# Performance work log

Measured on AMD Instinct MI355X. Metric: run time of the kernel, lower is better.

## Reference

```python
import jax, jax.numpy as jnp
import numpy as np

N_NODES = 100000
E_HALF = 500000   # undirected pairs; mirrored to E = 1M directed edges
NFEAT = 128
NHID = 64
NCLASS = 40


def setup_inputs() -> dict:
    key = jax.random.key(0)
    ks = jax.random.split(key, 8)
    s = jax.random.randint(ks[0], (E_HALF,), 0, N_NODES, dtype=jnp.int32)
    off = jax.random.randint(ks[1], (E_HALF,), 1, N_NODES, dtype=jnp.int32)
    d = (s + off) % N_NODES  # no self-loops in the raw edge list
    src = jnp.concatenate([s, d])
    dst = jnp.concatenate([d, s])
    ar = jnp.arange(E_HALF, dtype=jnp.int32)
    rev = jnp.concatenate([ar + E_HALF, ar])  # index of reverse edge (j,i) for edge (i,j)
    x = jax.random.uniform(ks[2], (N_NODES, NFEAT), dtype=jnp.float32)
    W1 = jax.random.normal(ks[3], (NFEAT, NHID), jnp.float32) / np.sqrt(NFEAT).astype(np.float32)
    b1 = jnp.zeros((NHID,), jnp.float32)
    W2 = jax.random.normal(ks[4], (NHID, NCLASS), jnp.float32) / np.sqrt(NHID).astype(np.float32)
    b2 = jnp.zeros((NCLASS,), jnp.float32)
    Wd = jax.random.normal(ks[5], (2, 1), jnp.float32)
    bd = jax.random.normal(ks[6], (1,), jnp.float32) * 0.1
    return {"x": x, "src": src, "dst": dst, "rev": rev,
            "W1": W1, "b1": b1, "W2": W2, "b2": b2, "Wd": Wd, "bd": bd}


def att_coef(f, src, dst, rev, n, Wd, bd, mask):
    """Edge-list version of GuardGCN.att_coef (drop=True).
    mask zeroes edges removed by a previous att_coef pass.
    Returns (per-edge weights [E], per-node self-loop weights [n])."""
    nrm = jnp.sqrt(jnp.sum(f * f, axis=1))
    safe = jnp.where(nrm == 0, 1.0, nrm)
    # cosine similarity only on the listed edges (diagonal handled via lam below)
    sim = jnp.sum(f[src] * f[dst], axis=1) / (safe[src] * safe[dst])
    sim = jnp.where(sim < 0.1, 0.0, sim) * mask
    # L1 row normalization (sklearn normalize(axis=1, norm='l1'))
    rowsum = jax.ops.segment_sum(jnp.abs(sim), src, num_segments=n)
    a = sim / jnp.where(rowsum == 0, 1.0, rowsum)[src]
    # learnable drop: Linear(2,1) on [a_ij, a_ji] -> sigmoid -> binary keep at 0.5
    char = jnp.stack([a, a[rev]], axis=1)  # [E, 2]
    keep = jax.nn.sigmoid(char @ Wd + bd)[:, 0] > 0.5
    a = jnp.where(keep, a, 0.0)
    # self-loop weight lam_i = 1 / (deg_i + 1), deg = surviving out-edges
    deg = jax.ops.segment_sum((a != 0).astype(f.dtype), src, num_segments=n)
    lam = 1.0 / (deg + 1.0)
    # exp() applied only to nonzero entries (zeros are absent in sparse nonzero())
    w_e = jnp.where(a > 0, jnp.exp(a), 0.0)
    w_s = jnp.exp(lam)
    return w_e, w_s


def gcn_conv(h, src, dst, w, n, W, b):
    """torch_geometric GCNConv: gcn_norm (add self-loops fill=1, sym D^-1/2 A D^-1/2),
    then aggregate h @ W along edges (src -> dst) and add bias."""
    h = h @ W
    iota = jnp.arange(n, dtype=src.dtype)
    src2 = jnp.concatenate([src, iota])
    dst2 = jnp.concatenate([dst, iota])
    w2 = jnp.concatenate([w, jnp.ones((n,), h.dtype)])
    deg = jax.ops.segment_sum(w2, dst2, num_segments=n)
    dis = jnp.where(deg > 0, deg ** -0.5, 0.0)
    norm = dis[src2] * w2 * dis[dst2]
    out = jax.ops.segment_sum(norm[:, None] * h[src2], dst2, num_segments=n)
    return out + b


def reference(x, src, dst, rev, W1, b1, W2, b2, Wd, bd):
    n = x.shape[0]
    iota = jnp.arange(n, dtype=src.dtype)
    # layer-0 attention on raw features
    w_e1, w_s1 = att_coef(x, src, dst, rev, n, Wd, bd, jnp.ones(src.shape, x.dtype))
    src_f = jnp.concatenate([src, iota])
    dst_f = jnp.concatenate([dst, iota])
    w_f1 = jnp.concatenate([w_e1, w_s1])
    h = jax.nn.relu(gcn_conv(x, src_f, dst_f, w_f1, n, W1, b1))
    # layer-1 attention on hidden features; edge set = survivors of pass 0
    mask1 = (w_e1 > 0).astype(x.dtype)
    w_e2, w_s2 = att_coef(h, src, dst, rev, n, Wd, bd, mask1)
    w_f2 = jnp.concatenate([w_e2, w_s2])
    # dropout is identity in eval mode
    out = gcn_conv(h, src_f, dst_f, w_f2, n, W2, b2)
    return jax.nn.log_softmax(out, axis=1)
```

## Files before the change

### kernel.cpp

```cpp
#include <hip/hip_runtime.h>

#define N_NODES 100000
#define E_HALF  500000
#define E_TOT   1000000
#define NFEAT   128
#define NHID    64
#define NCLS    40
#define NBUK    782
#define NSUB    8
#define CAP     448

__device__ __forceinline__ int REV(int e) { return (e < E_HALF) ? e + E_HALF : e - E_HALF; }

template<int D>
__global__ __launch_bounds__(256) void row_norm_k(const float* __restrict__ x, float* __restrict__ nrm) {
    int w = (blockIdx.x * 256 + threadIdx.x) >> 6;
    int lane = threadIdx.x & 63;
    if (w >= N_NODES) return;
    const float* row = x + (size_t)w * D;
    float s = 0.f;
#pragma unroll
    for (int i = 0; i < D / 64; ++i) { float v = row[lane + 64 * i]; s = fmaf(v, v, s); }
#pragma unroll
    for (int off = 32; off; off >>= 1) s += __shfl_xor(s, off);
    if (lane == 0) nrm[w] = sqrtf(s);
}

template<int D, int L, bool MASKED>
__global__ __launch_bounds__(256) void sim_k(const float* __restrict__ f, const float* __restrict__ nrm,
                                             const int* __restrict__ src, const int* __restrict__ dst,
                                             const float* __restrict__ we_mask,
                                             float* __restrict__ sim) {
    static_assert(D / L == 16, "each lane covers 16 floats");
    int g = blockIdx.x * 256 + threadIdx.x;
    int ep = g / L, sl = g % L;
    if (ep >= E_HALF) return;
    bool m0 = true, m1 = true;
    if (MASKED) {
        m0 = we_mask[ep] > 0.f;
        m1 = we_mask[ep + E_HALF] > 0.f;
        if (!m0 && !m1) {
            if (sl == 0) { sim[ep] = 0.f; sim[ep + E_HALF] = 0.f; }
            return;
        }
    }
    int s = src[ep], d = dst[ep];
    const float* fa = f + (size_t)s * D + sl * 16;
    const float* fb = f + (size_t)d * D + sl * 16;
    float acc = 0.f;
#pragma unroll
    for (int i = 0; i < 16; i += 4) {
        float4 va = *(const float4*)(fa + i);
        float4 vb = *(const float4*)(fb + i);
        acc = fmaf(va.x, vb.x, acc); acc = fmaf(va.y, vb.y, acc);
        acc = fmaf(va.z, vb.z, acc); acc = fmaf(va.w, vb.w, acc);
    }
#pragma unroll
    for (int off = L / 2; off; off >>= 1) acc += __shfl_xor(acc, off);
    if (sl == 0) {
        float na = nrm[s]; na = (na == 0.f) ? 1.f : na;
        float nb = nrm[d]; nb = (nb == 0.f) ? 1.f : nb;
        float c = acc / (na * nb);
        float t = (c < 0.1f) ? 0.f : c;
        sim[ep]          = m0 ? t : 0.f;
        sim[ep + E_HALF] = m1 ? t : 0.f;
    }
}

__global__ __launch_bounds__(256) void rowsum_k(const float* __restrict__ sim, const int* __restrict__ row_start,
                                                const int2* __restrict__ csr, float* __restrict__ rowsum) {
    int g = blockIdx.x * 256 + threadIdx.x;
    int j = g >> 2, l = g & 3;
    if (j >= N_NODES) return;
    int e0 = row_start[j], e1 = row_start[j + 1];
    float s = 0.f;
    for (int t = e0 + l; t < e1; t += 4) s += sim[csr[t].y];
    s += __shfl_xor(s, 1); s += __shfl_xor(s, 2);
    if (l == 0) rowsum[j] = s;
}

__global__ __launch_bounds__(256) void keep_k(const float* __restrict__ sim,
                                              const int* __restrict__ src, const int* __restrict__ dst,
                                              const float* __restrict__ rowsum,
                                              const float* __restrict__ Wd, const float* __restrict__ bd,
                                              float* __restrict__ we) {
    int e = blockIdx.x * 256 + threadIdx.x;
    if (e >= E_TOT) return;
    int s = src[e], d = dst[e];
    float rs = rowsum[s]; rs = (rs == 0.f) ? 1.f : rs;
    float rd = rowsum[d]; rd = (rd == 0.f) ? 1.f : rd;
    float ae = sim[e] / rs;
    float ar = sim[REV(e)] / rd;
    float z = ae * Wd[0] + ar * Wd[1] + bd[0];
    float av = (z > 0.f) ? ae : 0.f;
    we[e] = (av > 0.f) ? expf(av) : 0.f;
}

__global__ __launch_bounds__(256) void nodeB_k(const float* __restrict__ we, const int* __restrict__ row_start,
                                               const int2* __restrict__ csr,
                                               float* __restrict__ w_s, float* __restrict__ dis,
                                               float* __restrict__ wrev) {
    int g = blockIdx.x * 256 + threadIdx.x;
    int j = g >> 2, l = g & 3;
    if (j >= N_NODES) return;
    int e0 = row_start[j], e1 = row_start[j + 1];
    float c = 0.f, s = 0.f;
    for (int t = e0 + l; t < e1; t += 4) {
        int eid = csr[t].y;
        float wr = we[REV(eid)];
        wrev[t] = wr;
        c += (we[eid] > 0.f) ? 1.f : 0.f;
        s += wr;
    }
    c += __shfl_xor(c, 1); c += __shfl_xor(c, 2);
    s += __shfl_xor(s, 1); s += __shfl_xor(s, 2);
    if (l == 0) {
        float ws = expf(1.f / (c + 1.f));
        w_s[j] = ws;
        dis[j] = 1.f / sqrtf(s + ws + 1.f);
    }
}

__global__ __launch_bounds__(256) void fillA_k(const int* __restrict__ src, const int* __restrict__ dst,
                                               int* __restrict__ bcur, long long* __restrict__ stage) {
    int e = blockIdx.x * 256 + threadIdx.x;
    if (e >= E_TOT) return;
    int s = src[e];
    int buk = s >> 7;
    int sub = blockIdx.x & 7;
    int p = atomicAdd(&bcur[sub * NBUK + buk], 1);
    if (p < CAP) {
        long long pk = ((long long)e << 24) | ((long long)(s & 127) << 17) | (unsigned)dst[e];
        stage[((size_t)(sub * NBUK + buk)) * CAP + p] = pk;
    }
}

__global__ __launch_bounds__(256) void bukscan_k(const int* __restrict__ bcur, int* __restrict__ bbase) {
    __shared__ int part[256];
    int t = threadIdx.x;
    int loc[4]; int s = 0;
#pragma unroll
    for (int i = 0; i < 4; ++i) {
        int b = t * 4 + i; int c = 0;
        if (b < NBUK)
#pragma unroll
            for (int sub = 0; sub < NSUB; ++sub) c += min(bcur[sub * NBUK + b], CAP);
        loc[i] = c; s += c;
    }
    part[t] = s;
    __syncthreads();
    if (t == 0) { int run = 0; for (int k = 0; k < 256; ++k) { int v = part[k]; part[k] = run; run += v; } }
    __syncthreads();
    int base = part[t];
#pragma unroll
    for (int i = 0; i < 4; ++i) {
        int b = t * 4 + i;
        if (b < NBUK) { bbase[b] = base; base += loc[i]; }
    }
}

__global__ __launch_bounds__(256) void fillB_k(const long long* __restrict__ stage, const int* __restrict__ bcur,
                                               const int* __restrict__ bbase,
                                               int* __restrict__ row_start, int2* __restrict__ csr) {
    int buk = blockIdx.x;
    int n0 = buk << 7;
    __shared__ int lcnt[128], lofs[129], lcur[128];
    int t = threadIdx.x;
    if (t < 128) { lcnt[t] = 0; lcur[t] = 0; }
    __syncthreads();
    int cnts[NSUB];
#pragma unroll
    for (int sub = 0; sub < NSUB; ++sub) {
        int n = min(bcur[sub * NBUK + buk], CAP);
        cnts[sub] = n;
        const long long* sp = stage + ((size_t)(sub * NBUK + buk)) * CAP;
        for (int k = t; k < n; k += 256)
            atomicAdd(&lcnt[(int)((sp[k] >> 17) & 127)], 1);
    }
    __syncthreads();
    if (t == 0) { int run = 0; for (int i = 0; i < 128; ++i) { lofs[i] = run; run += lcnt[i]; } lofs[128] = run; }
    __syncthreads();
    int base = bbase[buk];
    if (t < 128 && n0 + t < N_NODES) row_start[n0 + t] = base + lofs[t];
    if (buk == NBUK - 1 && t == 0)   row_start[N_NODES] = base + lofs[128];
#pragma unroll
    for (int sub = 0; sub < NSUB; ++sub) {
        int n = cnts[sub];
        const long long* sp = stage + ((size_t)(sub * NBUK + buk)) * CAP;
        for (int k = t; k < n; k += 256) {
            long long pk = sp[k];
            int d17 = (int)(pk & 0x1FFFF);
            int slo = (int)((pk >> 17) & 127);
            int eid = (int)(pk >> 24);
            int r = atomicAdd(&lcur[slo], 1);
            csr[base + lofs[slo] + r] = make_int2(d17, eid);
        }
    }
}

__global__ __launch_bounds__(256) void gemm1_k(const float* __restrict__ X, const float* __restrict__ W,
                                               const float* __restrict__ dis, float* __restrict__ Y) {
    __shared__ float sXT[8][128];
    __shared__ float sW[8][64];
    int tid = threadIdx.x;
    int row0 = blockIdx.x * 128;
    int tc = tid & 15;
    int tr = tid >> 4;
    float acc[8][4] = {};
    int lrow = tid >> 1, lhalf = tid & 1;
    int grow = row0 + lrow;
    for (int k0 = 0; k0 < NFEAT; k0 += 8) {
        float4 v = make_float4(0.f, 0.f, 0.f, 0.f);
        if (grow < N_NODES) v = *(const float4*)(X + (size_t)grow * NFEAT + k0 + lhalf * 4);
        sXT[lhalf * 4 + 0][lrow] = v.x;
        sXT[lhalf * 4 + 1][lrow] = v.y;
        sXT[lhalf * 4 + 2][lrow] = v.z;
        sXT[lhalf * 4 + 3][lrow] = v.w;
        float2 wv2 = *(const float2*)(W + (size_t)(k0 + (tid >> 5)) * NHID + (tid & 31) * 2);
        *(float2*)&sW[tid >> 5][(tid & 31) * 2] = wv2;
        __syncthreads();
#pragma unroll
        for (int k = 0; k < 8; ++k) {
            float4 xa = *(const float4*)&sXT[k][tr * 8];
            float4 xb = *(const float4*)&sXT[k][tr * 8 + 4];
            float4 wv = *(const float4*)&sW[k][tc * 4];
            float xr[8] = {xa.x, xa.y, xa.z, xa.w, xb.x, xb.y, xb.z, xb.w};
            float wr[4] = {wv.x, wv.y, wv.z, wv.w};
#pragma unroll
            for (int i = 0; i < 8; ++i)
#pragma unroll
                for (int jj = 0; jj < 4; ++jj)
                    acc[i][jj] = fmaf(xr[i], wr[jj], acc[i][jj]);
        }
        __syncthreads();
    }
#pragma unroll
    for (int i = 0; i < 8; ++i) {
        int r = row0 + tr * 8 + i;
        if (r < N_NODES) {
            float dr = dis[r];
            *(float4*)(Y + (size_t)r * NHID + tc * 4) =
                make_float4(acc[i][0] * dr, acc[i][1] * dr, acc[i][2] * dr, acc[i][3] * dr);
        }
    }
}

__global__ __launch_bounds__(256) void gemm2_k(const float* __restrict__ X, const float* __restrict__ W,
                                               const float* __restrict__ dis, float* __restrict__ Y) {
    __shared__ float sXT[8][128];
    __shared__ float sW[320];
    int tid = threadIdx.x;
    int row0 = blockIdx.x * 128;
    int tc = tid & 7;
    int tr = tid >> 3;
    float acc[4][5] = {};
    int lrow = tid >> 1, lhalf = tid & 1;
    int grow = row0 + lrow;
    for (int k0 = 0; k0 < NHID; k0 += 8) {
        float4 v = make_float4(0.f, 0.f, 0.f, 0.f);
        if (grow < N_NODES) v = *(const float4*)(X + (size_t)grow * NHID + k0 + lhalf * 4);
        sXT[lhalf * 4 + 0][lrow] = v.x;
        sXT[lhalf * 4 + 1][lrow] = v.y;
        sXT[lhalf * 4 + 2][lrow] = v.z;
        sXT[lhalf * 4 + 3][lrow] = v.w;
        if (tid < 160) {
            float2 w2 = *(const float2*)(W + k0 * NCLS + tid * 2);
            sW[tid * 2] = w2.x; sW[tid * 2 + 1] = w2.y;
        }
        __syncthreads();
#pragma unroll
        for (int k = 0; k < 8; ++k) {
            float4 xv = *(const float4*)&sXT[k][tr * 4];
            float xr[4] = {xv.x, xv.y, xv.z, xv.w};
            float wr[5];
#pragma unroll
            for (int jj = 0; jj < 5; ++jj) wr[jj] = sW[k * NCLS + tc * 5 + jj];
#pragma unroll
            for (int i = 0; i < 4; ++i)
#pragma unroll
                for (int jj = 0; jj < 5; ++jj)
                    acc[i][jj] = fmaf(xr[i], wr[jj], acc[i][jj]);
        }
        __syncthreads();
    }
#pragma unroll
    for (int i = 0; i < 4; ++i) {
        int r = row0 + tr * 4 + i;
        if (r < N_NODES) {
            float dr = dis[r];
#pragma unroll
            for (int jj = 0; jj < 5; ++jj) Y[(size_t)r * NCLS + tc * 5 + jj] = acc[i][jj] * dr;
        }
    }
}

__global__ __launch_bounds__(256) void agg1_k(const float* __restrict__ hs, const int* __restrict__ row_start,
                                              const int2* __restrict__ csr, const float* __restrict__ wrev,
                                              const float* __restrict__ dis, const float* __restrict__ w_s,
                                              const float* __restrict__ b, float* __restrict__ h,
                                              float* __restrict__ nrm) {
    int j = (blockIdx.x * 256 + threadIdx.x) >> 6;
    int lane = threadIdx.x & 63;
    if (j >= N_NODES) return;
    int e0 = row_start[j], e1 = row_start[j + 1];
    float acc = 0.f;
    int t = e0;
    for (; t + 4 <= e1; t += 4) {
        int2 c0 = csr[t], c1 = csr[t + 1], c2 = csr[t + 2], c3 = csr[t + 3];
        float w0 = wrev[t], w1 = wrev[t + 1], w2 = wrev[t + 2], w3 = wrev[t + 3];
        float v0 = hs[(size_t)c0.x * NHID + lane];
        float v1 = hs[(size_t)c1.x * NHID + lane];
        float v2 = hs[(size_t)c2.x * NHID + lane];
        float v3 = hs[(size_t)c3.x * NHID + lane];
        acc = fmaf(w0, v0, acc); acc = fmaf(w1, v1, acc);
        acc = fmaf(w2, v2, acc); acc = fmaf(w3, v3, acc);
    }
    for (; t < e1; ++t)
        acc = fmaf(wrev[t], hs[(size_t)csr[t].x * NHID + lane], acc);
    acc = fmaf(w_s[j] + 1.f, hs[(size_t)j * NHID + lane], acc);
    float v = fmaxf(fmaf(acc, dis[j], b[lane]), 0.f);
    h[(size_t)j * NHID + lane] = v;
    float s = v * v;
#pragma unroll
    for (int off = 32; off; off >>= 1) s += __shfl_xor(s, off);
    if (lane == 0) nrm[j] = sqrtf(s);
}

__global__ __launch_bounds__(256) void agg2_k(const float* __restrict__ hs2, const int* __restrict__ row_start,
                                              const int2* __restrict__ csr, const float* __restrict__ wrev,
                                              const float* __restrict__ dis, const float* __restrict__ w_s,
                                              const float* __restrict__ b, float* __restrict__ out) {
    int j = (blockIdx.x * 256 + threadIdx.x) >> 6;
    int lane = threadIdx.x & 63;
    if (j >= N_NODES) return;
    int lc = (lane < NCLS) ? lane : (NCLS - 1);
    int e0 = row_start[j], e1 = row_start[j + 1];
    float acc = 0.f;
    int t = e0;
    for (; t + 4 <= e1; t += 4) {
        int2 c0 = csr[t], c1 = csr[t + 1], c2 = csr[t + 2], c3 = csr[t + 3];
        float w0 = wrev[t], w1 = wrev[t + 1], w2 = wrev[t + 2], w3 = wrev[t + 3];
        float v0 = hs2[(size_t)c0.x * NCLS + lc];
        float v1 = hs2[(size_t)c1.x * NCLS + lc];
        float v2 = hs2[(size_t)c2.x * NCLS + lc];
        float v3 = hs2[(size_t)c3.x * NCLS + lc];
        acc = fmaf(w0, v0, acc); acc = fmaf(w1, v1, acc);
        acc = fmaf(w2, v2, acc); acc = fmaf(w3, v3, acc);
    }
    for (; t < e1; ++t)
        acc = fmaf(wrev[t], hs2[(size_t)csr[t].x * NCLS + lc], acc);
    acc = fmaf(w_s[j] + 1.f, hs2[(size_t)j * NCLS + lc], acc);
    float v = (lane < NCLS) ? fmaf(acc, dis[j], b[lane]) : -1e30f;
    float m = v;
#pragma unroll
    for (int off = 32; off; off >>= 1) m = fmaxf(m, __shfl_xor(m, off));
    float ex = (lane < NCLS) ? expf(v - m) : 0.f;
    float ssum = ex;
#pragma unroll
    for (int off = 32; off; off >>= 1) ssum += __shfl_xor(ssum, off);
    if (lane < NCLS) out[(size_t)j * NCLS + lane] = v - m - logf(ssum);
}

extern "C" void kernel_launch(void* const* d_in, const int* in_sizes, int n_in,
                              void* d_out, int out_size, void* d_ws, size_t ws_size,
                              hipStream_t stream) {
    (void)in_sizes; (void)n_in; (void)out_size; (void)ws_size;
    const float* x  = (const float*)d_in[0];
    const int*   src = (const int*)d_in[1];
    const int*   dst = (const int*)d_in[2];
    const float* W1 = (const float*)d_in[4];
    const float* b1 = (const float*)d_in[5];
    const float* W2 = (const float*)d_in[6];
    const float* b2 = (const float*)d_in[7];
    const float* Wd = (const float*)d_in[8];
    const float* bd = (const float*)d_in[9];
    float* out = (float*)d_out;

    char* ws = (char*)d_ws;
    size_t off = 0;
    auto alloc = [&](size_t bytes) -> void* {
        void* p = ws + off;
        off = (off + bytes + 255) & ~(size_t)255;
        return p;
    };
    int*   bcur   = (int*)alloc((size_t)NSUB * NBUK * 4);
    int*   bbase  = (int*)alloc((size_t)NBUK * 4);
    float* nrm    = (float*)alloc((size_t)N_NODES * 4);
    float* rowsum = (float*)alloc((size_t)N_NODES * 4);
    float* w_s    = (float*)alloc((size_t)N_NODES * 4);
    float* dis    = (float*)alloc((size_t)N_NODES * 4);
    float* sbuf   = (float*)alloc((size_t)E_TOT * 4);
    float* we1    = (float*)alloc((size_t)E_TOT * 4);
    float* we2    = (float*)alloc((size_t)E_TOT * 4);
    float* wrev   = (float*)alloc((size_t)E_TOT * 4);
    float* hs     = (float*)alloc((size_t)N_NODES * NHID * 4);
    float* h      = (float*)alloc((size_t)N_NODES * NHID * 4);
    int*  row_start = (int*)alloc((size_t)(N_NODES + 1) * 4);
    int2* csr       = (int2*)alloc((size_t)E_TOT * 8);
    long long* stage = (long long*)hs;

    const int BE  = (E_TOT + 255) / 256;
    const int BW  = (N_NODES * 64 + 255) / 256;
    const int BQ  = (N_NODES * 4 + 255) / 256;
    const int BS8 = (E_HALF * 8 + 255) / 256;
    const int BS4 = (E_HALF * 4 + 255) / 256;
    const int BG  = (N_NODES + 127) / 128;

    hipMemsetAsync(bcur, 0, (size_t)NSUB * NBUK * 4, stream);
    fillA_k<<<BE, 256, 0, stream>>>(src, dst, bcur, stage);
    bukscan_k<<<1, 256, 0, stream>>>(bcur, bbase);
    fillB_k<<<NBUK, 256, 0, stream>>>(stage, bcur, bbase, row_start, csr);

    row_norm_k<NFEAT><<<BW, 256, 0, stream>>>(x, nrm);
    sim_k<NFEAT, 8, false><<<BS8, 256, 0, stream>>>(x, nrm, src, dst, nullptr, sbuf);
    rowsum_k<<<BQ, 256, 0, stream>>>(sbuf, row_start, csr, rowsum);
    keep_k<<<BE, 256, 0, stream>>>(sbuf, src, dst, rowsum, Wd, bd, we1);
    nodeB_k<<<BQ, 256, 0, stream>>>(we1, row_start, csr, w_s, dis, wrev);
    gemm1_k<<<BG, 256, 0, stream>>>(x, W1, dis, hs);
    agg1_k<<<BW, 256, 0, stream>>>(hs, row_start, csr, wrev, dis, w_s, b1, h, nrm);

    sim_k<NHID, 4, true><<<BS4, 256, 0, stream>>>(h, nrm, src, dst, we1, sbuf);
    rowsum_k<<<BQ, 256, 0, stream>>>(sbuf, row_start, csr, rowsum);
    keep_k<<<BE, 256, 0, stream>>>(sbuf, src, dst, rowsum, Wd, bd, we2);
    nodeB_k<<<BQ, 256, 0, stream>>>(we2, row_start, csr, w_s, dis, wrev);
    gemm2_k<<<BG, 256, 0, stream>>>(h, W2, dis, hs);
    agg2_k<<<BW, 256, 0, stream>>>(hs, row_start, csr, wrev, dis, w_s, b2, out);
}
```

Baseline: 544.3 us.

## Fuse row norms into similarity and keep decision into node pass

Removes the separate row-norm kernel by computing both squared norms inside the edge-pair similarity kernel from the already-loaded feature vectors. Stores layer-0 similarity once per undirected pair, exploiting symmetry. The keep/drop decision is folded into the per-node pass, which drops the keep kernel and the per-edge weight arrays; the layer-1 mask is recomputed from the stored pair similarity and row sums. This cuts two launches per layer and several 1M-edge array passes, at the cost of extra FMAs, shuffles and scattered row-sum reads.

```diff
diff --git a/kernel.cpp b/kernel.cpp
--- a/kernel.cpp
+++ b/kernel.cpp
@@ -11,64 +11,114 @@
 #define CAP     448
 
 __device__ __forceinline__ int REV(int e) { return (e < E_HALF) ? e + E_HALF : e - E_HALF; }
-
-template<int D>
-__global__ __launch_bounds__(256) void row_norm_k(const float* __restrict__ x, float* __restrict__ nrm) {
-    int w = (blockIdx.x * 256 + threadIdx.x) >> 6;
-    int lane = threadIdx.x & 63;
-    if (w >= N_NODES) return;
-    const float* row = x + (size_t)w * D;
-    float s = 0.f;
-#pragma unroll
-    for (int i = 0; i < D / 64; ++i) { float v = row[lane + 64 * i]; s = fmaf(v, v, s); }
-#pragma unroll
-    for (int off = 32; off; off >>= 1) s += __shfl_xor(s, off);
-    if (lane == 0) nrm[w] = sqrtf(s);
-}
-
-template<int D, int L, bool MASKED>
-__global__ __launch_bounds__(256) void sim_k(const float* __restrict__ f, const float* __restrict__ nrm,
-                                             const int* __restrict__ src, const int* __restrict__ dst,
-                                             const float* __restrict__ we_mask,
-                                             float* __restrict__ sim) {
-    static_assert(D / L == 16, "each lane covers 16 floats");
+__device__ __forceinline__ float guard0(float v) { return (v == 0.f) ? 1.f : v; }
+
+template<int D, int L>
+__global__ __launch_bounds__(256) void sim1_k(const float* __restrict__ f,
+                                              const int* __restrict__ src, const int* __restrict__ dst,
+                                              float* __restrict__ spair) {
+    static_assert(D / L == 16, "each lane covers 16 floats (one 64B line)");
     int g = blockIdx.x * 256 + threadIdx.x;
     int ep = g / L, sl = g % L;
     if (ep >= E_HALF) return;
-    bool m0 = true, m1 = true;
-    if (MASKED) {
-        m0 = we_mask[ep] > 0.f;
-        m1 = we_mask[ep + E_HALF] > 0.f;
-        if (!m0 && !m1) {
-            if (sl == 0) { sim[ep] = 0.f; sim[ep + E_HALF] = 0.f; }
-            return;
-        }
-    }
     int s = src[ep], d = dst[ep];
     const float* fa = f + (size_t)s * D + sl * 16;
     const float* fb = f + (size_t)d * D + sl * 16;
-    float acc = 0.f;
+    float dot = 0.f, na2 = 0.f, nb2 = 0.f;
 #pragma unroll
     for (int i = 0; i < 16; i += 4) {
         float4 va = *(const float4*)(fa + i);
         float4 vb = *(const float4*)(fb + i);
-        acc = fmaf(va.x, vb.x, acc); acc = fmaf(va.y, vb.y, acc);
-        acc = fmaf(va.z, vb.z, acc); acc = fmaf(va.w, vb.w, acc);
-    }
-#pragma unroll
-    for (int off = L / 2; off; off >>= 1) acc += __shfl_xor(acc, off);
+        dot = fmaf(va.x, vb.x, dot); dot = fmaf(va.y, vb.y, dot);
+        dot = fmaf(va.z, vb.z, dot); dot = fmaf(va.w, vb.w, dot);
+        na2 = fmaf(va.x, va.x, na2); na2 = fmaf(va.y, va.y, na2);
+        na2 = fmaf(va.z, va.z, na2); na2 = fmaf(va.w, va.w, na2);
+        nb2 = fmaf(vb.x, vb.x, nb2); nb2 = fmaf(vb.y, vb.y, nb2);
+        nb2 = fmaf(vb.z, vb.z, nb2); nb2 = fmaf(vb.w, vb.w, nb2);
+    }
+#pragma unroll
+    for (int off = L / 2; off; off >>= 1) {
+        dot += __shfl_xor(dot, off);
+        na2 += __shfl_xor(na2, off);
+        nb2 += __shfl_xor(nb2, off);
+    }
     if (sl == 0) {
-        float na = nrm[s]; na = (na == 0.f) ? 1.f : na;
-        float nb = nrm[d]; nb = (nb == 0.f) ? 1.f : nb;
-        float c = acc / (na * nb);
+        float na = guard0(sqrtf(na2));
+        float nb = guard0(sqrtf(nb2));
+        float c = dot / (na * nb);
+        spair[ep] = (c < 0.1f) ? 0.f : c;
+    }
+}
+
+template<int D, int L>
+__global__ __launch_bounds__(256) void sim2_k(const float* __restrict__ f,
+                                              const int* __restrict__ src, const int* __restrict__ dst,
+                                              const float* __restrict__ spair1, const float* __restrict__ rs1,
+                                              const float* __restrict__ Wd, const float* __restrict__ bd,
+                                              float* __restrict__ sim) {
+    static_assert(D / L == 16, "each lane covers 16 floats (one 64B line)");
+    int g = blockIdx.x * 256 + threadIdx.x;
+    int ep = g / L, sl = g % L;
+    if (ep >= E_HALF) return;
+    int s = src[ep], d = dst[ep];
+    float sp = spair1[ep];
+    float rsv = guard0(rs1[s]);
+    float rdv = guard0(rs1[d]);
+    float ae = sp / rsv, ar = sp / rdv;
+    float w0 = Wd[0], w1 = Wd[1], b0 = bd[0];
+    bool m0 = (ae * w0 + ar * w1 + b0 > 0.f) && (ae > 0.f);
+    bool m1 = (ar * w0 + ae * w1 + b0 > 0.f) && (ar > 0.f);
+    if (!m0 && !m1) {
+        if (sl == 0) { sim[ep] = 0.f; sim[ep + E_HALF] = 0.f; }
+        return;
+    }
+    const float* fa = f + (size_t)s * D + sl * 16;
+    const float* fb = f + (size_t)d * D + sl * 16;
+    float dot = 0.f, na2 = 0.f, nb2 = 0.f;
+#pragma unroll
+    for (int i = 0; i < 16; i += 4) {
+        float4 va = *(const float4*)(fa + i);
+        float4 vb = *(const float4*)(fb + i);
+        dot = fmaf(va.x, vb.x, dot); dot = fmaf(va.y, vb.y, dot);
+        dot = fmaf(va.z, vb.z, dot); dot = fmaf(va.w, vb.w, dot);
+        na2 = fmaf(va.x, va.x, na2); na2 = fmaf(va.y, va.y, na2);
+        na2 = fmaf(va.z, va.z, na2); na2 = fmaf(va.w, va.w, na2);
+        nb2 = fmaf(vb.x, vb.x, nb2); nb2 = fmaf(vb.y, vb.y, nb2);
+        nb2 = fmaf(vb.z, vb.z, nb2); nb2 = fmaf(vb.w, vb.w, nb2);
+    }
+#pragma unroll
+    for (int off = L / 2; off; off >>= 1) {
+        dot += __shfl_xor(dot, off);
+        na2 += __shfl_xor(na2, off);
+        nb2 += __shfl_xor(nb2, off);
+    }
+    if (sl == 0) {
+        float na = guard0(sqrtf(na2));
+        float nb = guard0(sqrtf(nb2));
+        float c = dot / (na * nb);
         float t = (c < 0.1f) ? 0.f : c;
         sim[ep]          = m0 ? t : 0.f;
         sim[ep + E_HALF] = m1 ? t : 0.f;
     }
 }
 
-__global__ __launch_bounds__(256) void rowsum_k(const float* __restrict__ sim, const int* __restrict__ row_start,
-                                                const int2* __restrict__ csr, float* __restrict__ rowsum) {
+__global__ __launch_bounds__(256) void rowsum1_k(const float* __restrict__ spair, const int* __restrict__ row_start,
+                                                 const int2* __restrict__ csr, float* __restrict__ rowsum) {
+    int g = blockIdx.x * 256 + threadIdx.x;
+    int j = g >> 2, l = g & 3;
+    if (j >= N_NODES) return;
+    int e0 = row_start[j], e1 = row_start[j + 1];
+    float s = 0.f;
+    for (int t = e0 + l; t < e1; t += 4) {
+        int y = csr[t].y;
+        s += spair[(y < E_HALF) ? y : y - E_HALF];
+    }
+    s += __shfl_xor(s, 1); s += __shfl_xor(s, 2);
+    if (l == 0) rowsum[j] = s;
+}
+
+__global__ __launch_bounds__(256) void rowsum2_k(const float* __restrict__ sim, const int* __restrict__ row_start,
+                                                 const int2* __restrict__ csr, float* __restrict__ rowsum) {
     int g = blockIdx.x * 256 + threadIdx.x;
     int j = g >> 2, l = g & 3;
     if (j >= N_NODES) return;
@@ -79,45 +129,70 @@
     if (l == 0) rowsum[j] = s;
 }
 
-__global__ __launch_bounds__(256) void keep_k(const float* __restrict__ sim,
-                                              const int* __restrict__ src, const int* __restrict__ dst,
-                                              const float* __restrict__ rowsum,
-                                              const float* __restrict__ Wd, const float* __restrict__ bd,
-                                              float* __restrict__ we) {
-    int e = blockIdx.x * 256 + threadIdx.x;
-    if (e >= E_TOT) return;
-    int s = src[e], d = dst[e];
-    float rs = rowsum[s]; rs = (rs == 0.f) ? 1.f : rs;
-    float rd = rowsum[d]; rd = (rd == 0.f) ? 1.f : rd;
-    float ae = sim[e] / rs;
-    float ar = sim[REV(e)] / rd;
-    float z = ae * Wd[0] + ar * Wd[1] + bd[0];
-    float av = (z > 0.f) ? ae : 0.f;
-    we[e] = (av > 0.f) ? expf(av) : 0.f;
-}
-
-__global__ __launch_bounds__(256) void nodeB_k(const float* __restrict__ we, const int* __restrict__ row_start,
-                                               const int2* __restrict__ csr,
-                                               float* __restrict__ w_s, float* __restrict__ dis,
-                                               float* __restrict__ wrev) {
+__global__ __launch_bounds__(256) void nodeB1_k(const float* __restrict__ spair, const int* __restrict__ row_start,
+                                                const int2* __restrict__ csr, const float* __restrict__ rs,
+                                                const float* __restrict__ Wd, const float* __restrict__ bd,
+                                                float* __restrict__ w_s, float* __restrict__ dis,
+                                                float* __restrict__ wrev) {
     int g = blockIdx.x * 256 + threadIdx.x;
     int j = g >> 2, l = g & 3;
     if (j >= N_NODES) return;
     int e0 = row_start[j], e1 = row_start[j + 1];
-    float c = 0.f, s = 0.f;
+    float rsj = guard0(rs[j]);
+    float w0 = Wd[0], w1 = Wd[1], b0 = bd[0];
+    float c = 0.f, ssum = 0.f;
     for (int t = e0 + l; t < e1; t += 4) {
-        int eid = csr[t].y;
-        float wr = we[REV(eid)];
+        int2 cc = csr[t];
+        int y = cc.y;
+        float sp = spair[(y < E_HALF) ? y : y - E_HALF];
+        float rscol = guard0(rs[cc.x]);
+        float ae = sp / rsj;
+        float ar = sp / rscol;
+        c += ((ae * w0 + ar * w1 + b0 > 0.f) && ae > 0.f) ? 1.f : 0.f;
+        float wr = ((ar * w0 + ae * w1 + b0 > 0.f) && ar > 0.f) ? expf(ar) : 0.f;
         wrev[t] = wr;
-        c += (we[eid] > 0.f) ? 1.f : 0.f;
-        s += wr;
+        ssum += wr;
     }
     c += __shfl_xor(c, 1); c += __shfl_xor(c, 2);
-    s += __shfl_xor(s, 1); s += __shfl_xor(s, 2);
+    ssum += __shfl_xor(ssum, 1); ssum += __shfl_xor(ssum, 2);
     if (l == 0) {
         float ws = expf(1.f / (c + 1.f));
         w_s[j] = ws;
-        dis[j] = 1.f / sqrtf(s + ws + 1.f);
+        dis[j] = 1.f / sqrtf(ssum + ws + 1.f);
+    }
+}
+
+__global__ __launch_bounds__(256) void nodeB2_k(const float* __restrict__ sim, const int* __restrict__ row_start,
+                                                const int2* __restrict__ csr, const float* __restrict__ rs,
+                                                const float* __restrict__ Wd, const float* __restrict__ bd,
+                                                float* __restrict__ w_s, float* __restrict__ dis,
+                                                float* __restrict__ wrev) {
+    int g = blockIdx.x * 256 + threadIdx.x;
+    int j = g >> 2, l = g & 3;
+    if (j >= N_NODES) return;
+    int e0 = row_start[j], e1 = row_start[j + 1];
+    float rsj = guard0(rs[j]);
+    float w0 = Wd[0], w1 = Wd[1], b0 = bd[0];
+    float c = 0.f, ssum = 0.f;
+    for (int t = e0 + l; t < e1; t += 4) {
+        int2 cc = csr[t];
+        int y = cc.y;
+        float s0 = sim[y];
+        float s1 = sim[REV(y)];
+        float rscol = guard0(rs[cc.x]);
+        float ae = s0 / rsj;
+        float ar = s1 / rscol;
+        c += ((ae * w0 + ar * w1 + b0 > 0.f) && ae > 0.f) ? 1.f : 0.f;
+        float wr = ((ar * w0 + ae * w1 + b0 > 0.f) && ar > 0.f) ? expf(ar) : 0.f;
+        wrev[t] = wr;
+        ssum += wr;
+    }
+    c += __shfl_xor(c, 1); c += __shfl_xor(c, 2);
+    ssum += __shfl_xor(ssum, 1); ssum += __shfl_xor(ssum, 2);
+    if (l == 0) {
+        float ws = expf(1.f / (c + 1.f));
+        w_s[j] = ws;
+        dis[j] = 1.f / sqrtf(ssum + ws + 1.f);
     }
 }
 
@@ -297,8 +372,7 @@
 __global__ __launch_bounds__(256) void agg1_k(const float* __restrict__ hs, const int* __restrict__ row_start,
                                               const int2* __restrict__ csr, const float* __restrict__ wrev,
                                               const float* __restrict__ dis, const float* __restrict__ w_s,
-                                              const float* __restrict__ b, float* __restrict__ h,
-                                              float* __restrict__ nrm) {
+                                              const float* __restrict__ b, float* __restrict__ h) {
     int j = (blockIdx.x * 256 + threadIdx.x) >> 6;
     int lane = threadIdx.x & 63;
     if (j >= N_NODES) return;
@@ -318,12 +392,7 @@
     for (; t < e1; ++t)
         acc = fmaf(wrev[t], hs[(size_t)csr[t].x * NHID + lane], acc);
     acc = fmaf(w_s[j] + 1.f, hs[(size_t)j * NHID + lane], acc);
-    float v = fmaxf(fmaf(acc, dis[j], b[lane]), 0.f);
-    h[(size_t)j * NHID + lane] = v;
-    float s = v * v;
-#pragma unroll
-    for (int off = 32; off; off >>= 1) s += __shfl_xor(s, off);
-    if (lane == 0) nrm[j] = sqrtf(s);
+    h[(size_t)j * NHID + lane] = fmaxf(fmaf(acc, dis[j], b[lane]), 0.f);
 }
 
 __global__ __launch_bounds__(256) void agg2_k(const float* __restrict__ hs2, const int* __restrict__ row_start,
@@ -385,13 +454,12 @@
     };
     int*   bcur   = (int*)alloc((size_t)NSUB * NBUK * 4);
     int*   bbase  = (int*)alloc((size_t)NBUK * 4);
-    float* nrm    = (float*)alloc((size_t)N_NODES * 4);
-    float* rowsum = (float*)alloc((size_t)N_NODES * 4);
+    float* rs1    = (float*)alloc((size_t)N_NODES * 4);
+    float* rs2    = (float*)alloc((size_t)N_NODES * 4);
     float* w_s    = (float*)alloc((size_t)N_NODES * 4);
     float* dis    = (float*)alloc((size_t)N_NODES * 4);
-    float* sbuf   = (float*)alloc((size_t)E_TOT * 4);
-    float* we1    = (float*)alloc((size_t)E_TOT * 4);
-    float* we2    = (float*)alloc((size_t)E_TOT * 4);
+    float* spair  = (float*)alloc((size_t)E_HALF * 4);
+    float* sbuf2  = (float*)alloc((size_t)E_TOT * 4);
     float* wrev   = (float*)alloc((size_t)E_TOT * 4);
     float* hs     = (float*)alloc((size_t)N_NODES * NHID * 4);
     float* h      = (float*)alloc((size_t)N_NODES * NHID * 4);
@@ -399,9 +467,9 @@
     int2* csr       = (int2*)alloc((size_t)E_TOT * 8);
     long long* stage = (long long*)hs;
 
-    const int BE  = (E_TOT + 255) / 256;
     const int BW  = (N_NODES * 64 + 255) / 256;
     const int BQ  = (N_NODES * 4 + 255) / 256;
+    const int BE  = (E_TOT + 255) / 256;
     const int BS8 = (E_HALF * 8 + 255) / 256;
     const int BS4 = (E_HALF * 4 + 255) / 256;
     const int BG  = (N_NODES + 127) / 128;
@@ -411,18 +479,15 @@
     bukscan_k<<<1, 256, 0, stream>>>(bcur, bbase);
     fillB_k<<<NBUK, 256, 0, stream>>>(stage, bcur, bbase, row_start, csr);
 
-    row_norm_k<NFEAT><<<BW, 256, 0, stream>>>(x, nrm);
-    sim_k<NFEAT, 8, false><<<BS8, 256, 0, stream>>>(x, nrm, src, dst, nullptr, sbuf);
-    rowsum_k<<<BQ, 256, 0, stream>>>(sbuf, row_start, csr, rowsum);
-    keep_k<<<BE, 256, 0, stream>>>(sbuf, src, dst, rowsum, Wd, bd, we1);
-    nodeB_k<<<BQ, 256, 0, stream>>>(we1, row_start, csr, w_s, dis, wrev);
+    sim1_k<NFEAT, 8><<<BS8, 256, 0, stream>>>(x, src, dst, spair);
+    rowsum1_k<<<BQ, 256, 0, stream>>>(spair, row_start, csr, rs1);
+    nodeB1_k<<<BQ, 256, 0, stream>>>(spair, row_start, csr, rs1, Wd, bd, w_s, dis, wrev);
     gemm1_k<<<BG, 256, 0, stream>>>(x, W1, dis, hs);
-    agg1_k<<<BW, 256, 0, stream>>>(hs, row_start, csr, wrev, dis, w_s, b1, h, nrm);
-
-    sim_k<NHID, 4, true><<<BS4, 256, 0, stream>>>(h, nrm, src, dst, we1, sbuf);
-    rowsum_k<<<BQ, 256, 0, stream>>>(sbuf, row_start, csr, rowsum);
-    keep_k<<<BE, 256, 0, stream>>>(sbuf, src, dst, rowsum, Wd, bd, we2);
-    nodeB_k<<<BQ, 256, 0, stream>>>(we2, row_start, csr, w_s, dis, wrev);
+    agg1_k<<<BW, 256, 0, stream>>>(hs, row_start, csr, wrev, dis, w_s, b1, h);
+
+    sim2_k<NHID, 4><<<BS4, 256, 0, stream>>>(h, src, dst, spair, rs1, Wd, bd, sbuf2);
+    rowsum2_k<<<BQ, 256, 0, stream>>>(sbuf2, row_start, csr, rs2);
+    nodeB2_k<<<BQ, 256, 0, stream>>>(sbuf2, row_start, csr, rs2, Wd, bd, w_s, dis, wrev);
     gemm2_k<<<BG, 256, 0, stream>>>(h, W2, dis, hs);
     agg2_k<<<BW, 256, 0, stream>>>(hs, row_start, csr, wrev, dis, w_s, b2, out);
 }
```

Result: faster. 495.0 us (-9.1%).
